# Performance work log

Hardware: AMD Instinct MI355X
Metric: run time of the kernel (lower is better)

## Reference

```python
import jax, jax.numpy as jnp
import numpy as np

N_NODES = 100000
N_EDGES = 1600000
IN_DIM = 500
HID = 32
N_REL = 7
OUT_DIM = 4
N_GRAPHS = 16


def setup_inputs() -> dict:
    key = jax.random.key(0)
    ks = jax.random.split(key, 9)
    node_x = jax.random.normal(ks[0], (N_NODES, IN_DIM), dtype=jnp.float32)
    edge_index = jax.random.randint(ks[1], (2, N_EDGES), 0, N_NODES, dtype=jnp.int64)
    edge_attr = jax.random.randint(ks[2], (N_EDGES,), 0, N_REL, dtype=jnp.int64)
    batch = jnp.sort(jax.random.randint(ks[3], (N_NODES,), 0, N_GRAPHS, dtype=jnp.int64))
    # learned params (RGCNConv: per-relation weight, root weight, bias; then fc)
    s_in = 1.0 / np.sqrt(IN_DIM)
    W_rel = jax.random.uniform(ks[4], (N_REL, IN_DIM, HID), jnp.float32, -s_in, s_in)
    W_root = jax.random.uniform(ks[5], (IN_DIM, HID), jnp.float32, -s_in, s_in)
    bias = jnp.zeros((HID,), jnp.float32)
    s_h = 1.0 / np.sqrt(HID)
    fc_w = jax.random.uniform(ks[6], (HID, OUT_DIM), jnp.float32, -s_h, s_h)
    fc_b = jax.random.uniform(ks[7], (OUT_DIM,), jnp.float32, -s_h, s_h)
    return {"node_x": node_x, "edge_index": edge_index, "edge_attr": edge_attr,
            "batch": batch, "W_rel": W_rel, "W_root": W_root, "bias": bias,
            "fc_w": fc_w, "fc_b": fc_b}


def _rgcn(node_x, edge_index, edge_attr, W_rel, W_root, bias):
    # PyG RGCNConv with default aggr='mean': per-relation mean over incoming
    # edges, summed across relations, plus root transform and bias.
    src, dst = edge_index[0], edge_index[1]
    out = node_x @ W_root + bias  # [N, HID]
    for r in range(N_REL):
        h = node_x @ W_rel[r]                       # [N, HID] transform first (cheap: HID << IN_DIM)
        m = (edge_attr == r).astype(node_x.dtype)   # [E] relation mask
        msg = h[src] * m[:, None]                   # [E, HID]
        s = jax.ops.segment_sum(msg, dst, num_segments=N_NODES)
        cnt = jax.ops.segment_sum(m, dst, num_segments=N_NODES)
        out = out + s / jnp.maximum(cnt, 1.0)[:, None]
    return out


def reference(node_x, edge_index, edge_attr, batch, W_rel, W_root, bias, fc_w, fc_b):
    x = _rgcn(node_x, edge_index, edge_attr, W_rel, W_root, bias)
    x = jax.nn.relu(x)
    # global_add_pool over per-node graph ids
    pooled = jax.ops.segment_sum(x, batch, num_segments=N_GRAPHS)  # [B, HID]
    return pooled @ fc_w + fc_b  # [B, OUT_DIM]
```

## Files before the change

kernel.cpp:

```cpp
#include <hip/hip_runtime.h>

#define N_NODES 100000
#define N_EDGES 1600000
#define IN_DIM 500
#define HID 32
#define N_REL 7
#define OUT_DIM 4
#define N_GRAPHS 16
#define NC 256
#define MC 224
#define KPAD 512

#define BK_SHIFT 6
#define BK_NODES 64
#define N_BUCKETS ((N_NODES + BK_NODES - 1) / BK_NODES)
#define NSUB 8
#define SUB_CAP 256
#define BK_CAP (NSUB * SUB_CAP)
#define NPOOL 8

#define GEMM_BLOCKS 3125
#define BIN_BLOCKS  ((N_EDGES + 255) / 256)
#define N_GROUPS 1173
#define GRID_MERGED (N_GROUPS * 8)

typedef __attribute__((ext_vector_type(8))) short bf16x8;
typedef __attribute__((ext_vector_type(4))) float f32x4;

__device__ inline unsigned short f2bf(float f) {
    unsigned u = __float_as_uint(f);
    unsigned r = (u + 0x7FFFu + ((u >> 16) & 1u)) >> 16;
    return (unsigned short)r;
}
__device__ inline float bf2f(unsigned short b) {
    return __uint_as_float((unsigned)b << 16);
}

__global__ void build_wbf(const float* __restrict__ W_root,
                          const float* __restrict__ W_rel,
                          unsigned short* __restrict__ Wbf,
                          int* __restrict__ bcur,
                          float* __restrict__ pooled) {
    int idx = blockIdx.x * blockDim.x + threadIdx.x;
    if (idx < N_BUCKETS * NSUB) bcur[idx] = idx * SUB_CAP;
    if (idx < NPOOL * N_GRAPHS * HID) pooled[idx] = 0.f;
    if (idx >= KPAD * NC) return;
    int kk = idx >> 8;
    int n = idx & 255;
    float v = 0.f;
    if (kk < IN_DIM) {
        if (n < HID) v = W_root[kk * HID + n];
        else {
            int r = (n >> 5) - 1;
            v = W_rel[((size_t)r * IN_DIM + kk) * HID + (n & 31)];
        }
    }
    int ks = kk >> 5, q = (kk >> 3) & 3, j = kk & 7;
    Wbf[(size_t)((((ks << 2) + q) << 8) + n) * 8 + j] = f2bf(v);
}

__global__ __launch_bounds__(256, 6) void gemm_bin(const float* __restrict__ A,
                                                   const uint4* __restrict__ Wbf,
                                                   float* __restrict__ Hr,
                                                   unsigned short* __restrict__ Hm,
                                                   const int* __restrict__ src,
                                                   const int* __restrict__ dst,
                                                   const int* __restrict__ attr,
                                                   int* __restrict__ bcur,
                                                   int* __restrict__ rec) {
    const int grp = blockIdx.x >> 3, j8 = blockIdx.x & 7;

    if (grp % 3 != 0) {
        int bb = (grp - grp / 3 - 1) * 8 + j8;
        if (bb >= BIN_BLOCKS) return;
        int e = bb * 256 + threadIdx.x;
        if (e >= N_EDGES) return;
        int d = dst[e];
        int cur = (d >> BK_SHIFT) * NSUB + j8;
        int p = atomicAdd(&bcur[cur], 1);
        if (p < (cur + 1) * SUB_CAP)
            rec[p] = ((d & (BK_NODES - 1)) << 20) | (src[e] << 3) | attr[e];
        return;
    }

    int bid = (grp / 3) * 8 + j8;
    if (bid >= GEMM_BLOCKS) return;

    __shared__ uint4 Alds[32 * 32];

    const int tid = threadIdx.x;
    const int wave = tid >> 6, lane = tid & 63;
    const int l16 = lane & 15, q = lane >> 4;
    const int row0 = bid * 32;
    const int wn = wave * 64;

    const float4* Ablk4 = (const float4*)(A + (size_t)row0 * IN_DIM);

    f32x4 acc[2][4];
    #pragma unroll
    for (int mt = 0; mt < 2; mt++)
        #pragma unroll
        for (int nt = 0; nt < 4; nt++)
            #pragma unroll
            for (int r = 0; r < 4; r++) acc[mt][nt][r] = 0.f;

    for (int half = 0; half < 2; half++) {
        if (half) __syncthreads();
        #pragma unroll 4
        for (int it = 0; it < 8; it++) {
            int idx = it * 256 + tid;
            int row = idx >> 6, slot = idx & 63;
            int k = half * 256 + slot * 4;
            float4 v = make_float4(0.f, 0.f, 0.f, 0.f);
            if (k < IN_DIM)
                v = Ablk4[row * 125 + (k >> 2)];
            int ksq = slot >> 1;
            int e = (ksq << 5) | ((row ^ ksq) & 31);
            ushort4 b;
            b.x = f2bf(v.x); b.y = f2bf(v.y); b.z = f2bf(v.z); b.w = f2bf(v.w);
            *(ushort4*)((unsigned short*)&Alds[e] + (slot & 1) * 4) = b;
        }
        __syncthreads();
        #pragma unroll 2
        for (int ksl = 0; ksl < 8; ksl++) {
            int ksq_l = ksl * 4 + q;
            int ksq_g = half * 32 + ksq_l;
            bf16x8 bfr[4], afr[2];
            #pragma unroll
            for (int nt = 0; nt < 4; nt++) {
                uint4 t = Wbf[(size_t)(ksq_g << 8) + wn + nt * 16 + l16];
                bfr[nt] = *(bf16x8*)&t;
            }
            #pragma unroll
            for (int mt = 0; mt < 2; mt++)
                afr[mt] = *(const bf16x8*)&Alds[(ksq_l << 5) | (((mt * 16 + l16) ^ ksq_l) & 31)];
            #pragma unroll
            for (int mt = 0; mt < 2; mt++)
                #pragma unroll
                for (int nt = 0; nt < 4; nt++)
                    acc[mt][nt] = __builtin_amdgcn_mfma_f32_16x16x32_bf16(
                        afr[mt], bfr[nt], acc[mt][nt], 0, 0, 0);
        }
    }

    #pragma unroll
    for (int mt = 0; mt < 2; mt++) {
        int rbase = row0 + mt * 16 + q * 4;
        #pragma unroll
        for (int r = 0; r < 4; r++) {
            int row = rbase + r;
            #pragma unroll
            for (int nt = 0; nt < 4; nt++) {
                int col = wn + nt * 16 + l16;
                float v = acc[mt][nt][r];
                if (wave == 0 && nt < 2)
                    Hr[(size_t)row * HID + col] = v;
                else
                    Hm[(size_t)row * MC + (col - HID)] = f2bf(v);
            }
        }
    }
}

__global__ __launch_bounds__(256) void bucket_sort(int* __restrict__ rec,
                                                   const int* __restrict__ bcur,
                                                   int* __restrict__ deg,
                                                   int* __restrict__ offs,
                                                   float* __restrict__ invcnt) {
    __shared__ int h2[BK_NODES * N_REL];
    __shared__ int lcur[BK_NODES];
    __shared__ int sorted[BK_CAP];
    __shared__ int scnt[NSUB];
    __shared__ int s_total;

    const int b = blockIdx.x, t = threadIdx.x;
    const int n0 = b << BK_SHIFT;
    const size_t rbase = (size_t)b * BK_CAP;

    for (int i = t; i < BK_NODES * N_REL; i += 256) h2[i] = 0;
    if (t < NSUB) {
        int c = bcur[b * NSUB + t] - (b * NSUB + t) * SUB_CAP;
        scnt[t] = c < SUB_CAP ? c : SUB_CAP;
    }
    __syncthreads();

    for (int s = 0; s < NSUB; s++) {
        int cs = scnt[s];
        const int* rp = rec + rbase + s * SUB_CAP;
        for (int i = t; i < cs; i += 256) {
            int q = rp[i];
            atomicAdd(&h2[(q >> 20) * N_REL + (q & 7)], 1);
        }
    }
    __syncthreads();

    if (t < BK_NODES) {
        int tot = 0;
        #pragma unroll
        for (int r = 0; r < N_REL; r++) tot += h2[t * N_REL + r];
        int incl = tot;
        #pragma unroll
        for (int off = 1; off < BK_NODES; off <<= 1) {
            int y = __shfl_up(incl, off, 64);
            if (t >= off) incl += y;
        }
        int excl = incl - tot;
        lcur[t] = excl;
        if (t == BK_NODES - 1) s_total = incl;
        int n = n0 + t;
        if (n < N_NODES) {
            deg[n] = tot;
            offs[n] = (int)rbase + excl;
        }
    }
    int lim = (N_NODES - n0) * N_REL;
    if (lim > BK_NODES * N_REL) lim = BK_NODES * N_REL;
    for (int i = t; i < lim; i += 256) {
        int cc = h2[i];
        invcnt[(size_t)n0 * N_REL + i] = 1.0f / (float)(cc > 1 ? cc : 1);
    }
    __syncthreads();

    for (int s = 0; s < NSUB; s++) {
        int cs = scnt[s];
        const int* rp = rec + rbase + s * SUB_CAP;
        for (int i = t; i < cs; i += 256) {
            int q = rp[i];
            int p = atomicAdd(&lcur[q >> 20], 1);
            if (p < BK_CAP)
                sorted[p] = q & 0xFFFFF;
        }
    }
    __syncthreads();

    int total = s_total;
    if (total > BK_CAP) total = BK_CAP;
    for (int i = t; i < total; i += 256) rec[rbase + i] = sorted[i];
}

__global__ __launch_bounds__(256) void gather_agg(const int* __restrict__ rec,
                                                  const int* __restrict__ offs,
                                                  const int* __restrict__ deg,
                                                  const float* __restrict__ invcnt,
                                                  const float* __restrict__ bias,
                                                  const unsigned short* __restrict__ Hm,
                                                  const float* __restrict__ Hr,
                                                  const int* __restrict__ batch,
                                                  float* __restrict__ pooled) {
    __shared__ float lpool[N_GRAPHS][HID];
    const int t = threadIdx.x;
    for (int i = t; i < N_GRAPHS * HID; i += 256) ((float*)lpool)[i] = 0.f;
    __syncthreads();

    const int d = blockIdx.x * 8 + (t >> 5);
    const int c = t & 31;

    int dg = deg[d];
    int start = offs[d];
    int end = start + dg;

    float acc = 0.f;
    for (int i = start; i < end; i += 8) {
        int q[8];
        float h[8], w[8];
        #pragma unroll
        for (int j = 0; j < 8; j++) {
            bool ok = (i + j) < end;
            int qq = rec[i + j];
            q[j] = ok ? qq : 0;
            w[j] = ok ? 1.f : 0.f;
        }
        #pragma unroll
        for (int j = 0; j < 8; j++)
            h[j] = bf2f(Hm[(size_t)((q[j] >> 3) & 0x1FFFF) * MC + (q[j] & 7) * HID + c]);
        #pragma unroll
        for (int j = 0; j < 8; j++)
            acc = fmaf(h[j], w[j] * invcnt[d * N_REL + (q[j] & 7)], acc);
    }

    float v = Hr[(size_t)d * HID + c] + bias[c] + acc;
    v = fmaxf(v, 0.f);
    atomicAdd(&lpool[batch[d]][c], v);
    __syncthreads();

    float* pp = pooled + (size_t)(blockIdx.x & (NPOOL - 1)) * N_GRAPHS * HID;
    for (int i2 = t; i2 < N_GRAPHS * HID; i2 += 256) {
        float v2 = ((float*)lpool)[i2];
        if (v2 != 0.f) atomicAdd(&pp[i2], v2);
    }
}

__global__ void fc_kernel(const float* __restrict__ pooled, const float* __restrict__ fc_w,
                          const float* __restrict__ fc_b, float* __restrict__ out) {
    int t = threadIdx.x;
    if (t >= N_GRAPHS * OUT_DIM) return;
    int g = t >> 2, o = t & 3;
    float acc = fc_b[o];
    #pragma unroll
    for (int c = 0; c < HID; c++) {
        float p = 0.f;
        #pragma unroll
        for (int k = 0; k < NPOOL; k++)
            p += pooled[(size_t)(k * N_GRAPHS + g) * HID + c];
        acc += p * fc_w[c * OUT_DIM + o];
    }
    out[t] = acc;
}

extern "C" void kernel_launch(void* const* d_in, const int* in_sizes, int n_in,
                              void* d_out, int out_size, void* d_ws, size_t ws_size,
                              hipStream_t stream) {
    const float* node_x  = (const float*)d_in[0];
    const int*   edge_ix = (const int*)d_in[1];
    const int*   e_attr  = (const int*)d_in[2];
    const int*   batch   = (const int*)d_in[3];
    const float* W_rel   = (const float*)d_in[4];
    const float* W_root  = (const float*)d_in[5];
    const float* bias    = (const float*)d_in[6];
    const float* fc_w    = (const float*)d_in[7];
    const float* fc_b    = (const float*)d_in[8];
    float* out = (float*)d_out;

    char* ws = (char*)d_ws;
    size_t off = 0;
    auto alloc = [&](size_t bytes) {
        char* p = ws + off;
        off += (bytes + 255) & ~(size_t)255;
        return p;
    };
    unsigned short* Wbf = (unsigned short*)alloc((size_t)KPAD * NC * 2);
    float* Hr      = (float*)alloc((size_t)N_NODES * HID * 4);
    unsigned short* Hm = (unsigned short*)alloc((size_t)N_NODES * MC * 2);
    int*   rec     = (int*)  alloc((size_t)N_BUCKETS * BK_CAP * 4);
    int*   bcur    = (int*)  alloc((size_t)N_BUCKETS * NSUB * 4);
    int*   deg     = (int*)  alloc((size_t)N_NODES * 4);
    int*   offsb   = (int*)  alloc((size_t)N_NODES * 4);
    float* invcnt  = (float*)alloc((size_t)N_NODES * N_REL * 4);
    float* pooled  = (float*)alloc((size_t)NPOOL * N_GRAPHS * HID * 4);
    (void)ws_size; (void)in_sizes; (void)n_in; (void)out_size;

    const int* src = edge_ix;
    const int* dst = edge_ix + N_EDGES;

    build_wbf<<<(KPAD * NC + 255) / 256, 256, 0, stream>>>(W_root, W_rel, Wbf,
                                                           bcur, pooled);

    gemm_bin<<<GRID_MERGED, 256, 0, stream>>>(node_x, (const uint4*)Wbf, Hr, Hm,
                                              src, dst, e_attr, bcur, rec);

    bucket_sort<<<N_BUCKETS, 256, 0, stream>>>(rec, bcur, deg, offsb, invcnt);

    gather_agg<<<(N_NODES + 7) / 8, 256, 0, stream>>>(rec, offsb, deg, invcnt,
                                                      bias, Hm, Hr, batch, pooled);

    fc_kernel<<<1, 64, 0, stream>>>(pooled, fc_w, fc_b, out);
}
```

Before: 432.6 us.

## Load A fragments directly from global into MFMA registers, dropping LDS staging

The GEMM part of the fused kernel no longer stages the bf16-converted A tile through shared memory with barriers. Each wave now loads its own A fragments straight from global memory, converts them in registers, and feeds them to the MFMA instructions inside a fully unrolled K loop. K offsets past the end of the input are clamped to a valid address; the matching weights are zero-padded, so those lanes contribute nothing. This removes LDS traffic and syncs, but every wave now reads the same A rows, quadrupling L1/L2 requests, and launch bounds occupancy drops from 6 to 4 to leave room for more registers.

```diff
diff --git a/kernel.cpp b/kernel.cpp
--- a/kernel.cpp
+++ b/kernel.cpp
@@ -34,6 +34,15 @@
 }
 __device__ inline float bf2f(unsigned short b) {
     return __uint_as_float((unsigned)b << 16);
+}
+
+__device__ inline bf16x8 pack8(float4 lo, float4 hi) {
+    union { unsigned u[4]; bf16x8 v; } r;
+    r.u[0] = ((unsigned)f2bf(lo.y) << 16) | f2bf(lo.x);
+    r.u[1] = ((unsigned)f2bf(lo.w) << 16) | f2bf(lo.z);
+    r.u[2] = ((unsigned)f2bf(hi.y) << 16) | f2bf(hi.x);
+    r.u[3] = ((unsigned)f2bf(hi.w) << 16) | f2bf(hi.z);
+    return r.v;
 }
 
 __global__ void build_wbf(const float* __restrict__ W_root,
@@ -59,7 +68,7 @@
     Wbf[(size_t)((((ks << 2) + q) << 8) + n) * 8 + j] = f2bf(v);
 }
 
-__global__ __launch_bounds__(256, 6) void gemm_bin(const float* __restrict__ A,
+__global__ __launch_bounds__(256, 4) void gemm_bin(const float* __restrict__ A,
                                                    const uint4* __restrict__ Wbf,
                                                    float* __restrict__ Hr,
                                                    unsigned short* __restrict__ Hm,
@@ -86,15 +95,15 @@
     int bid = (grp / 3) * 8 + j8;
     if (bid >= GEMM_BLOCKS) return;
 
-    __shared__ uint4 Alds[32 * 32];
-
     const int tid = threadIdx.x;
     const int wave = tid >> 6, lane = tid & 63;
     const int l16 = lane & 15, q = lane >> 4;
     const int row0 = bid * 32;
     const int wn = wave * 64;
 
-    const float4* Ablk4 = (const float4*)(A + (size_t)row0 * IN_DIM);
+    const float* Ar0 = A + (size_t)(row0 + l16) * IN_DIM;
+    const float* Ar1 = Ar0 + 16 * IN_DIM;
+    const int kb = q * 8;
 
     f32x4 acc[2][4];
     #pragma unroll
@@ -104,43 +113,31 @@
             #pragma unroll
             for (int r = 0; r < 4; r++) acc[mt][nt][r] = 0.f;
 
-    for (int half = 0; half < 2; half++) {
-        if (half) __syncthreads();
-        #pragma unroll 4
-        for (int it = 0; it < 8; it++) {
-            int idx = it * 256 + tid;
-            int row = idx >> 6, slot = idx & 63;
-            int k = half * 256 + slot * 4;
-            float4 v = make_float4(0.f, 0.f, 0.f, 0.f);
-            if (k < IN_DIM)
-                v = Ablk4[row * 125 + (k >> 2)];
-            int ksq = slot >> 1;
-            int e = (ksq << 5) | ((row ^ ksq) & 31);
-            ushort4 b;
-            b.x = f2bf(v.x); b.y = f2bf(v.y); b.z = f2bf(v.z); b.w = f2bf(v.w);
-            *(ushort4*)((unsigned short*)&Alds[e] + (slot & 1) * 4) = b;
-        }
-        __syncthreads();
-        #pragma unroll 2
-        for (int ksl = 0; ksl < 8; ksl++) {
-            int ksq_l = ksl * 4 + q;
-            int ksq_g = half * 32 + ksq_l;
-            bf16x8 bfr[4], afr[2];
-            #pragma unroll
-            for (int nt = 0; nt < 4; nt++) {
-                uint4 t = Wbf[(size_t)(ksq_g << 8) + wn + nt * 16 + l16];
-                bfr[nt] = *(bf16x8*)&t;
-            }
-            #pragma unroll
-            for (int mt = 0; mt < 2; mt++)
-                afr[mt] = *(const bf16x8*)&Alds[(ksq_l << 5) | (((mt * 16 + l16) ^ ksq_l) & 31)];
-            #pragma unroll
-            for (int mt = 0; mt < 2; mt++)
-                #pragma unroll
-                for (int nt = 0; nt < 4; nt++)
-                    acc[mt][nt] = __builtin_amdgcn_mfma_f32_16x16x32_bf16(
-                        afr[mt], bfr[nt], acc[mt][nt], 0, 0, 0);
-        }
+    #pragma unroll
+    for (int ksq = 0; ksq < 16; ksq++) {
+        int kbase = ksq * 32 + kb;
+        int o0 = kbase <= 496 ? kbase : 496;
+        int o1 = kbase + 4 <= 496 ? kbase + 4 : 496;
+        float4 a00 = *(const float4*)(Ar0 + o0);
+        float4 a01 = *(const float4*)(Ar0 + o1);
+        float4 a10 = *(const float4*)(Ar1 + o0);
+        float4 a11 = *(const float4*)(Ar1 + o1);
+        bf16x8 bfr[4];
+        #pragma unroll
+        for (int nt = 0; nt < 4; nt++) {
+            uint4 t = Wbf[(size_t)((((ksq << 2) | q)) << 8) + wn + nt * 16 + l16];
+            bfr[nt] = *(bf16x8*)&t;
+        }
+        bf16x8 afr0 = pack8(a00, a01);
+        bf16x8 afr1 = pack8(a10, a11);
+        #pragma unroll
+        for (int nt = 0; nt < 4; nt++)
+            acc[0][nt] = __builtin_amdgcn_mfma_f32_16x16x32_bf16(
+                afr0, bfr[nt], acc[0][nt], 0, 0, 0);
+        #pragma unroll
+        for (int nt = 0; nt < 4; nt++)
+            acc[1][nt] = __builtin_amdgcn_mfma_f32_16x16x32_bf16(
+                afr1, bfr[nt], acc[1][nt], 0, 0, 0);
     }
 
     #pragma unroll
```

Result: slower. 511.1 us (+18.1%).

## Stream fp32 A tile directly into LDS and convert to bf16 at fragment load

Applied to the files above, without the earlier changes.

The GEMM's A-tile staging no longer goes through registers. Each wave now copies fp32 rows straight from global memory into LDS with global_load_lds, using an XOR swizzle on the 16-byte segment index. The bf16 conversion moves to fragment-read time through the packed v_cvt_pk_bf16_f32 instruction, and the out-of-range tail segments are clamped to valid addresses because the padded weight rows are zero. The LDS tile doubles in size and occupancy is lowered to 4 blocks per SIMD, trading residency for less VGPR staging and fewer per-element conversion instructions on the load path.

```diff
diff --git a/kernel.cpp b/kernel.cpp
--- a/kernel.cpp
+++ b/kernel.cpp
@@ -59,7 +59,7 @@
     Wbf[(size_t)((((ks << 2) + q) << 8) + n) * 8 + j] = f2bf(v);
 }
 
-__global__ __launch_bounds__(256, 6) void gemm_bin(const float* __restrict__ A,
+__global__ __launch_bounds__(256, 4) void gemm_bin(const float* __restrict__ A,
                                                    const uint4* __restrict__ Wbf,
                                                    float* __restrict__ Hr,
                                                    unsigned short* __restrict__ Hm,
@@ -86,7 +86,7 @@
     int bid = (grp / 3) * 8 + j8;
     if (bid >= GEMM_BLOCKS) return;
 
-    __shared__ uint4 Alds[32 * 32];
+    __shared__ float4 AldsG[32 * 64];
 
     const int tid = threadIdx.x;
     const int wave = tid >> 6, lane = tid & 63;
@@ -94,8 +94,6 @@
     const int row0 = bid * 32;
     const int wn = wave * 64;
 
-    const float4* Ablk4 = (const float4*)(A + (size_t)row0 * IN_DIM);
-
     f32x4 acc[2][4];
     #pragma unroll
     for (int mt = 0; mt < 2; mt++)
@@ -106,40 +104,46 @@
 
     for (int half = 0; half < 2; half++) {
         if (half) __syncthreads();
-        #pragma unroll 4
+        #pragma unroll
         for (int it = 0; it < 8; it++) {
-            int idx = it * 256 + tid;
-            int row = idx >> 6, slot = idx & 63;
-            int k = half * 256 + slot * 4;
-            float4 v = make_float4(0.f, 0.f, 0.f, 0.f);
-            if (k < IN_DIM)
-                v = Ablk4[row * 125 + (k >> 2)];
-            int ksq = slot >> 1;
-            int e = (ksq << 5) | ((row ^ ksq) & 31);
-            ushort4 b;
-            b.x = f2bf(v.x); b.y = f2bf(v.y); b.z = f2bf(v.z); b.w = f2bf(v.w);
-            *(ushort4*)((unsigned short*)&Alds[e] + (slot & 1) * 4) = b;
+            int row = wave * 8 + it;
+            int s = row & 7;
+            int sg = lane ^ s;
+            if (half) sg = sg < 60 ? sg : 60;
+            const float* gp = A + (size_t)(row0 + row) * IN_DIM + half * 256 + sg * 4;
+            __builtin_amdgcn_global_load_lds(
+                (const __attribute__((address_space(1))) void*)gp,
+                (__attribute__((address_space(3))) void*)&AldsG[row * 64],
+                16, 0, 0);
         }
         __syncthreads();
         #pragma unroll 2
         for (int ksl = 0; ksl < 8; ksl++) {
-            int ksq_l = ksl * 4 + q;
-            int ksq_g = half * 32 + ksq_l;
-            bf16x8 bfr[4], afr[2];
+            int K = ksl * 4 + q;
+            int ksq_g = half * 32 + K;
+            bf16x8 bfr[4];
             #pragma unroll
             for (int nt = 0; nt < 4; nt++) {
                 uint4 t = Wbf[(size_t)(ksq_g << 8) + wn + nt * 16 + l16];
                 bfr[nt] = *(bf16x8*)&t;
             }
             #pragma unroll
-            for (int mt = 0; mt < 2; mt++)
-                afr[mt] = *(const bf16x8*)&Alds[(ksq_l << 5) | (((mt * 16 + l16) ^ ksq_l) & 31)];
-            #pragma unroll
-            for (int mt = 0; mt < 2; mt++)
+            for (int mt = 0; mt < 2; mt++) {
+                int row = mt * 16 + l16;
+                int s = row & 7;
+                int g0 = (2 * K) ^ s;
+                float4 fa = *(const float4*)&AldsG[row * 64 + g0];
+                float4 fb = *(const float4*)&AldsG[row * 64 + (g0 ^ 1)];
+                union { unsigned u[4]; bf16x8 v; } af;
+                asm("v_cvt_pk_bf16_f32 %0, %1, %2" : "=v"(af.u[0]) : "v"(fa.x), "v"(fa.y));
+                asm("v_cvt_pk_bf16_f32 %0, %1, %2" : "=v"(af.u[1]) : "v"(fa.z), "v"(fa.w));
+                asm("v_cvt_pk_bf16_f32 %0, %1, %2" : "=v"(af.u[2]) : "v"(fb.x), "v"(fb.y));
+                asm("v_cvt_pk_bf16_f32 %0, %1, %2" : "=v"(af.u[3]) : "v"(fb.z), "v"(fb.w));
                 #pragma unroll
                 for (int nt = 0; nt < 4; nt++)
                     acc[mt][nt] = __builtin_amdgcn_mfma_f32_16x16x32_bf16(
-                        afr[mt], bfr[nt], acc[mt][nt], 0, 0, 0);
+                        af.v, bfr[nt], acc[mt][nt], 0, 0, 0);
+            }
         }
     }
 
```

Measured after the change: 408.8 us. 5.5% less time.
